# Performance work log

Hardware: AMD Instinct MI355X
Metric: run time of the kernel (lower is better)

Reference implementation:

```python
import jax, jax.numpy as jnp
import numpy as np

K = 20           # top_k
EPS_NORM = 1e-12  # F.normalize default eps


def setup_inputs() -> dict:
    key = jax.random.key(0)
    ks = jax.random.split(key, 16)
    B, C, R, S, SCB, ST, H = 8192, 3755, 214, 13, 30, 6, 64
    return {
        "char_logits": jax.random.normal(ks[0], (B, C), jnp.float32),
        "radical_logits": jax.random.normal(ks[1], (B, R), jnp.float32),
        "structure": jax.random.normal(ks[2], (B, S), jnp.float32),
        "stroke_count": jax.random.normal(ks[3], (B, SCB), jnp.float32),
        "stroke_types": jax.random.normal(ks[4], (B, ST), jnp.float32),
        "radical_mask": jax.random.randint(ks[5], (C, R), 0, 2, jnp.int32),
        "structure_label": jax.random.randint(ks[6], (C,), 0, S, jnp.int32),
        "stroke_count_label": jax.random.randint(ks[7], (C,), 0, SCB, jnp.int32),
        "stroke_type_sig": jax.random.uniform(ks[8], (C, ST), jnp.float32),
        "W1": jax.random.normal(ks[9], (6, H), jnp.float32) * 0.3,
        "b1": jax.random.normal(ks[10], (H,), jnp.float32) * 0.1,
        "W2": jax.random.normal(ks[11], (H, 1), jnp.float32) * 0.3,
        "b2": jax.random.normal(ks[12], (1,), jnp.float32) * 0.1,
        "reranker_weight": jnp.asarray(0.1, jnp.float32),
    }


def _features(char_logits, radical_logits, structure, stroke_count, stroke_types,
              radical_mask, structure_label, stroke_count_label, stroke_type_sig,
              top_idx):
    sg = jax.lax.stop_gradient
    # all model outputs except char_logits are detached by caller; char_logits
    # is detached inside _compute_features for the neural-confidence feature
    rl, st, sc, sty = sg(radical_logits), sg(structure), sg(stroke_count), sg(stroke_types)
    cl_d = sg(char_logits)

    # feature 1/2: radical match & false-alarm ratios
    radical_probs = jax.nn.sigmoid(rl)                              # (B, R)
    cand_mask = radical_mask[top_idx].astype(jnp.float32)           # (B, K, R)
    detected = jnp.einsum('br,bkr->bk', radical_probs, cand_mask)   # (B, K)
    cand_counts = jnp.maximum(cand_mask.sum(-1), 1.0)
    radical_match_ratio = detected / cand_counts
    total_prob = jnp.maximum(radical_probs.sum(-1, keepdims=True), 1e-6)  # (B,1)
    false_alarm_mass = radical_probs.sum(-1, keepdims=True) - detected
    radical_false_ratio = false_alarm_mass / total_prob

    # feature 3: structure match probability
    structure_probs = jax.nn.softmax(st, axis=-1)                   # (B, S)
    cand_structure = structure_label[top_idx]                       # (B, K)
    structure_match = jnp.take_along_axis(structure_probs, cand_structure, axis=1)

    # feature 4: normalized stroke-count distance
    stroke_pred = jnp.argmax(sc, axis=-1)                           # (B,)
    cand_stroke = stroke_count_label[top_idx]                       # (B, K)
    stroke_distance = jnp.abs(stroke_pred[:, None] - cand_stroke).astype(jnp.float32) / 29.0

    # feature 5: zero-masked stroke-type cosine
    cand_sig = stroke_type_sig[top_idx]                             # (B, K, 6)
    sig_norm_val = jnp.linalg.norm(cand_sig, axis=-1)               # (B, K)
    has_sig = (sig_norm_val > 1e-6).astype(jnp.float32)
    pred_norm = sty / jnp.maximum(jnp.linalg.norm(sty, axis=-1, keepdims=True), EPS_NORM)
    cand_adj = cand_sig + 1e-8 * (1.0 - has_sig)[..., None]
    cand_norm = cand_adj / jnp.maximum(jnp.linalg.norm(cand_adj, axis=-1, keepdims=True), EPS_NORM)
    stroke_type_cos = jnp.einsum('bd,bkd->bk', pred_norm, cand_norm) * has_sig

    # feature 6: detached neural confidence
    neural_probs = jax.nn.softmax(cl_d, axis=-1)                    # (B, C)
    neural_conf = jnp.take_along_axis(neural_probs, top_idx, axis=1)

    return jnp.stack([radical_match_ratio, radical_false_ratio, structure_match,
                      stroke_distance, stroke_type_cos, neural_conf], axis=-1)  # (B, K, 6)


def reference(char_logits, radical_logits, structure, stroke_count, stroke_types,
              radical_mask, structure_label, stroke_count_label, stroke_type_sig,
              W1, b1, W2, b2, reranker_weight):
    B = char_logits.shape[0]
    top_logits, top_idx = jax.lax.top_k(char_logits, K)             # (B, K)
    feats = _features(char_logits, radical_logits, structure, stroke_count,
                      stroke_types, radical_mask, structure_label,
                      stroke_count_label, stroke_type_sig, top_idx)
    h = jax.nn.relu(feats @ W1 + b1)                                # (B, K, H)
    rerank_scores = (h @ W2 + b2)[..., 0]                           # (B, K)
    combined_top = top_logits + reranker_weight * rerank_scores
    rows = jnp.arange(B)[:, None]
    return char_logits.at[rows, top_idx].set(combined_top)
```

## Files before the change

### kernel.cpp

```cpp
#include <hip/hip_runtime.h>
#include <math.h>

#define NB   8192
#define NC   3755
#define NR   214
#define NS   13
#define NSC  30
#define NST  6
#define NH   64
#define KTOP 20
#define RPB  4
#define NT   (RPB * 64)
#define NQT  15
#define NBIN 1024
#define CAP  192

__device__ __forceinline__ unsigned sortkey(float x) {
    unsigned u = __float_as_uint(x);
    return (u & 0x80000000u) ? ~u : (u | 0x80000000u);
}
__device__ __forceinline__ float inv_sortkey(unsigned k) {
    unsigned u = (k & 0x80000000u) ? (k ^ 0x80000000u) : ~k;
    return __uint_as_float(u);
}
__device__ __forceinline__ int lane_prefix(unsigned long long m) {
    int c = __builtin_amdgcn_mbcnt_lo((unsigned)m, 0);
    return __builtin_amdgcn_mbcnt_hi((unsigned)(m >> 32), c);
}

__global__ __launch_bounds__(256) void prep_kernel(
    const int* __restrict__ radical_mask,
    unsigned*  __restrict__ ws_bits)
{
    const int lane = threadIdx.x & 63;
    const int wave = threadIdx.x >> 6;
    const int c    = blockIdx.x * 4 + wave;
    if (c >= NC) return;
    unsigned long long bits[4];
#pragma unroll
    for (int i = 0; i < 4; ++i) {
        int r = lane + i * 64;
        bool pred = (r < NR) && (radical_mask[(size_t)c * NR + r] != 0);
        bits[i] = __ballot(pred);
    }
    if (lane == 0) {
        uint4 wa = make_uint4((unsigned)bits[0], (unsigned)(bits[0] >> 32),
                              (unsigned)bits[1], (unsigned)(bits[1] >> 32));
        uint4 wb = make_uint4((unsigned)bits[2], (unsigned)(bits[2] >> 32),
                              (unsigned)bits[3], (unsigned)(bits[3] >> 32));
        reinterpret_cast<uint4*>(ws_bits)[(size_t)c * 2 + 0] = wa;
        reinterpret_cast<uint4*>(ws_bits)[(size_t)c * 2 + 1] = wb;
    }
}

__global__ __launch_bounds__(NT, 8) void select_kernel(
    const float* __restrict__ char_logits,
    float*       __restrict__ out,
    float*       __restrict__ ws_topv,
    int*         __restrict__ ws_topi,
    float*       __restrict__ ws_stat)
{
    const int tid  = threadIdx.x;
    const int lane = tid & 63;
    const int wave = tid >> 6;
    const int row  = blockIdx.x * RPB + wave;

    __shared__ unsigned           s_hist32[RPB / 2][NBIN];
    __shared__ unsigned long long s_cand[RPB][CAP];
    __shared__ int s_cnt[RPB];
    __shared__ int s_need[RPB];

    const int      hw  = wave >> 1;
    const unsigned hsh = (wave & 1) * 16;

    const size_t rowOff = (size_t)row * NC;
    const float* __restrict__ rin  = char_logits + rowOff;
    float*       __restrict__ rout = out + rowOff;

    const int a     = (int)((4 - (rowOff & 3)) & 3);
    const int nq    = (NC - a) >> 2;
    const int ntail = NC - a - 4 * nq;

    int ext_idx = -1;
    if (lane < a)                           ext_idx = lane;
    else if (lane >= 8 && lane < 8 + ntail) ext_idx = a + 4 * nq + (lane - 8);

    const unsigned FLOORK = 0xC0000000u;
    float ext = -INFINITY;
    if (ext_idx >= 0) {
        ext = rin[ext_idx];
        rout[ext_idx] = ext;
    }
    float e0 = __expf(ext), e1 = 0.f, e2 = 0.f, e3 = 0.f;
    float m0 = ext, m1 = -INFINITY, m2 = -INFINITY, m3 = -INFINITY;
    int base = 0;

#pragma unroll
    for (int t = 0; t < 14; ++t) {
        const int q = lane + t * 64;
        float4 x = *reinterpret_cast<const float4*>(rin + a + 4 * q);
        *reinterpret_cast<float4*>(rout + a + 4 * q) = x;
        e0 += __expf(x.x); e1 += __expf(x.y);
        e2 += __expf(x.z); e3 += __expf(x.w);
        m0 = fmaxf(m0, x.x); m1 = fmaxf(m1, x.y);
        m2 = fmaxf(m2, x.z); m3 = fmaxf(m3, x.w);
        unsigned kk[4] = { sortkey(x.x), sortkey(x.y), sortkey(x.z), sortkey(x.w) };
#pragma unroll
        for (int j = 0; j < 4; ++j) {
            bool pred = kk[j] >= FLOORK;
            unsigned long long bal = __ballot(pred);
            if (pred) {
                int pos = base + lane_prefix(bal);
                if (pos < CAP)
                    s_cand[wave][pos] = ((unsigned long long)kk[j] << 32)
                                      | (0xFFFFFFFFu - (unsigned)(a + 4 * q + j));
            }
            base += (int)__popcll(bal);
        }
    }
    {
        const int q = lane + 896;
        const bool inb = q < nq;
        float4 x = make_float4(-INFINITY, -INFINITY, -INFINITY, -INFINITY);
        if (inb) {
            x = *reinterpret_cast<const float4*>(rin + a + 4 * q);
            *reinterpret_cast<float4*>(rout + a + 4 * q) = x;
        }
        e0 += __expf(x.x); e1 += __expf(x.y);
        e2 += __expf(x.z); e3 += __expf(x.w);
        m0 = fmaxf(m0, x.x); m1 = fmaxf(m1, x.y);
        m2 = fmaxf(m2, x.z); m3 = fmaxf(m3, x.w);
        unsigned kk[4] = { sortkey(x.x), sortkey(x.y), sortkey(x.z), sortkey(x.w) };
#pragma unroll
        for (int j = 0; j < 4; ++j) {
            bool pred = kk[j] >= FLOORK;
            unsigned long long bal = __ballot(pred);
            if (pred) {
                int pos = base + lane_prefix(bal);
                if (pos < CAP)
                    s_cand[wave][pos] = ((unsigned long long)kk[j] << 32)
                                      | (0xFFFFFFFFu - (unsigned)(a + 4 * q + j));
            }
            base += (int)__popcll(bal);
        }
    }
    {
        unsigned k = sortkey(ext);
        bool pred = k >= FLOORK;
        unsigned long long bal = __ballot(pred);
        if (pred) {
            int pos = base + lane_prefix(bal);
            if (pos < CAP)
                s_cand[wave][pos] = ((unsigned long long)k << 32)
                                  | (0xFFFFFFFFu - (unsigned)ext_idx);
        }
        base += (int)__popcll(bal);
    }

    float lmax = fmaxf(fmaxf(m0, m1), fmaxf(m2, m3));
#pragma unroll
    for (int off = 32; off > 0; off >>= 1) lmax = fmaxf(lmax, __shfl_xor(lmax, off));
    const float rowmax = lmax;
    float S = (e0 + e1) + (e2 + e3);
#pragma unroll
    for (int off = 32; off > 0; off >>= 1) S += __shfl_xor(S, off);

    int M = base;
    const bool ok = (M >= KTOP) && (M <= CAP) && (fabsf(rowmax) <= 60.f);
    float sumexp = S * __expf(-rowmax);
    if (lane == 0) s_need[wave] = ok ? 0 : 1;
    __syncthreads();
    const int any = s_need[0] | s_need[1] | s_need[2] | s_need[3];

    if (any) {
        const bool bad = !ok;
        for (int i = tid; i < (RPB / 2) * NBIN; i += NT)
            (&s_hist32[0][0])[i] = 0u;
        __syncthreads();
        if (bad) {
            if (ext_idx >= 0) atomicAdd(&s_hist32[hw][sortkey(ext) >> 22], 1u << hsh);
            for (int t = 0; t < NQT; ++t) {
                int q = lane + t * 64;
                if (q < nq) {
                    float4 x = *reinterpret_cast<const float4*>(rin + a + 4 * q);
                    atomicAdd(&s_hist32[hw][sortkey(x.x) >> 22], 1u << hsh);
                    atomicAdd(&s_hist32[hw][sortkey(x.y) >> 22], 1u << hsh);
                    atomicAdd(&s_hist32[hw][sortkey(x.z) >> 22], 1u << hsh);
                    atomicAdd(&s_hist32[hw][sortkey(x.w) >> 22], 1u << hsh);
                }
            }
        }
        __syncthreads();
        int B0 = 0;
        if (bad) {
            int bb = (int)(sortkey(rowmax) >> 22), cum = 0;
            while (bb >= 0) {
                cum += (int)((s_hist32[hw][bb] >> hsh) & 0xFFFFu);
                if (cum >= KTOP) break;
                --bb;
            }
            B0 = (bb < 0) ? 0 : bb;
            if (lane == 0) s_cnt[wave] = 0;
        }
        __syncthreads();
        if (bad) {
            float f0 = 0.f, f1 = 0.f, f2 = 0.f, f3 = 0.f;
            if (ext_idx >= 0) {
                f0 += __expf(ext - rowmax);
                unsigned k = sortkey(ext);
                if ((int)(k >> 22) >= B0) {
                    int pos = atomicAdd(&s_cnt[wave], 1);
                    if (pos < CAP)
                        s_cand[wave][pos] = ((unsigned long long)k << 32) | (0xFFFFFFFFu - (unsigned)ext_idx);
                }
            }
            for (int t = 0; t < NQT; ++t) {
                int q = lane + t * 64;
                if (q < nq) {
                    float4 x = *reinterpret_cast<const float4*>(rin + a + 4 * q);
                    f0 += __expf(x.x - rowmax); f1 += __expf(x.y - rowmax);
                    f2 += __expf(x.z - rowmax); f3 += __expf(x.w - rowmax);
                    unsigned kk[4] = { sortkey(x.x), sortkey(x.y), sortkey(x.z), sortkey(x.w) };
#pragma unroll
                    for (int j = 0; j < 4; ++j) {
                        if ((int)(kk[j] >> 22) >= B0) {
                            int pos = atomicAdd(&s_cnt[wave], 1);
                            if (pos < CAP)
                                s_cand[wave][pos] = ((unsigned long long)kk[j] << 32)
                                                  | (0xFFFFFFFFu - (unsigned)(a + 4 * q + j));
                        }
                    }
                }
            }
            float ls = (f0 + f1) + (f2 + f3);
#pragma unroll
            for (int off = 32; off > 0; off >>= 1) ls += __shfl_xor(ls, off);
            sumexp = ls;
            M = s_cnt[wave]; if (M > CAP) M = CAP;
        }
    }

    for (int c = lane; c < M; c += 64) {
        unsigned long long pc = s_cand[wave][c];
        int rank = 0;
        for (int j = 0; j < M; ++j) rank += (s_cand[wave][j] > pc) ? 1 : 0;
        if (rank < KTOP) {
            ws_topv[(size_t)row * KTOP + rank] = inv_sortkey((unsigned)(pc >> 32));
            ws_topi[(size_t)row * KTOP + rank] = (int)(0xFFFFFFFFu - (unsigned)(pc & 0xFFFFFFFFu));
        }
    }
    if (lane == 0) {
        ws_stat[2 * row + 0] = rowmax;
        ws_stat[2 * row + 1] = sumexp;
    }
}

__global__ __launch_bounds__(256, 8) void rerank_kernel(
    const float* __restrict__ radical_logits,
    const float* __restrict__ structure,
    const float* __restrict__ stroke_count,
    const float* __restrict__ stroke_types,
    const int*   __restrict__ structure_label,
    const int*   __restrict__ stroke_count_label,
    const float* __restrict__ stroke_type_sig,
    const float* __restrict__ W1,
    const float* __restrict__ b1,
    const float* __restrict__ W2,
    const float* __restrict__ b2,
    const float* __restrict__ rw,
    const float* __restrict__ ws_topv,
    const int*   __restrict__ ws_topi,
    const float* __restrict__ ws_stat,
    const unsigned* __restrict__ ws_bits,
    float*       __restrict__ out)
{
    const int row  = blockIdx.x;
    const int tid  = threadIdx.x;
    const int lane = tid & 63;
    const int wave = tid >> 6;

    __shared__ float s_probs[256];
    __shared__ float s_struct[NS];
    __shared__ float s_aux[8];
    __shared__ float s_topv[KTOP];
    __shared__ int   s_topi[KTOP];
    __shared__ float s_stat2[2];

    s_probs[tid] = (tid < NR)
        ? 1.f / (1.f + __expf(-radical_logits[(size_t)row * NR + tid])) : 0.f;
    if (tid < KTOP) {
        s_topv[tid] = ws_topv[(size_t)row * KTOP + tid];
        s_topi[tid] = ws_topi[(size_t)row * KTOP + tid];
    }
    if (tid == 216) {
        float sv[NS]; float m = -INFINITY;
#pragma unroll
        for (int i = 0; i < NS; ++i) { sv[i] = structure[(size_t)row * NS + i]; m = fmaxf(m, sv[i]); }
        float s = 0.f;
#pragma unroll
        for (int i = 0; i < NS; ++i) { sv[i] = __expf(sv[i] - m); s += sv[i]; }
        float inv = 1.f / s;
#pragma unroll
        for (int i = 0; i < NS; ++i) s_struct[i] = sv[i] * inv;
    } else if (tid == 217) {
        float bv = -INFINITY; int bi = 0;
#pragma unroll
        for (int i = 0; i < NSC; ++i) {
            float x = stroke_count[(size_t)row * NSC + i];
            if (x > bv) { bv = x; bi = i; }
        }
        s_aux[6] = (float)bi;
    } else if (tid == 218) {
        float t6[NST]; float ss = 0.f;
#pragma unroll
        for (int i = 0; i < NST; ++i) { t6[i] = stroke_types[(size_t)row * NST + i]; ss += t6[i] * t6[i]; }
        float inv = 1.f / fmaxf(sqrtf(ss), 1e-12f);
#pragma unroll
        for (int i = 0; i < NST; ++i) s_aux[i] = t6[i] * inv;
    } else if (tid == 219) {
        s_stat2[0] = ws_stat[2 * row + 0];
        s_stat2[1] = ws_stat[2 * row + 1];
    }
    __syncthreads();

    const float p0 = s_probs[lane];
    const float p1 = s_probs[lane + 64];
    const float p2 = s_probs[lane + 128];
    const float p3 = s_probs[lane + 192];
    float psum = p0 + p1 + p2 + p3;
#pragma unroll
    for (int off = 32; off > 0; off >>= 1) psum += __shfl_xor(psum, off);
    const float total = psum;

    const float rowmax = s_stat2[0];
    const float sumexp = s_stat2[1];
    const float b1v = b1[lane];
    float w1v[6];
#pragma unroll
    for (int j = 0; j < 6; ++j) w1v[j] = W1[j * NH + lane];
    const float w2v = W2[lane];
    const float b2v = b2[0];
    const float wrk = rw[0];
    const float spred = s_aux[6];
    const unsigned l5 = lane & 31;
    const bool hi = lane >= 32;

#pragma unroll
    for (int j = 0; j < KTOP / 4; ++j) {
        const int   k  = wave * (KTOP / 4) + j;
        const int   ci = __builtin_amdgcn_readfirstlane(s_topi[k]);
        const float tv = s_topv[k];

        const uint4* bq = reinterpret_cast<const uint4*>(ws_bits) + (size_t)ci * 2;
        const uint4 wa = bq[0], wb = bq[1];
        float cnt = (float)(__popc(wa.x) + __popc(wa.y) + __popc(wa.z) + __popc(wa.w)
                          + __popc(wb.x) + __popc(wb.y) + __popc(wb.z));
        float det = 0.f;
        det += ((( hi ? wa.y : wa.x) >> l5) & 1u) ? p0 : 0.f;
        det += ((( hi ? wa.w : wa.z) >> l5) & 1u) ? p1 : 0.f;
        det += ((( hi ? wb.y : wb.x) >> l5) & 1u) ? p2 : 0.f;
        det += ((( hi ? wb.w : wb.z) >> l5) & 1u) ? p3 : 0.f;
#pragma unroll
        for (int off = 32; off > 0; off >>= 1) det += __shfl_xor(det, off);

        float f1 = det / fmaxf(cnt, 1.f);
        float f2 = (total - det) / fmaxf(total, 1e-6f);
        float f3 = s_struct[structure_label[ci]];
        float f4 = fabsf(spred - (float)stroke_count_label[ci]) * (1.f / 29.f);
        float sig[NST]; float ss = 0.f;
#pragma unroll
        for (int i = 0; i < NST; ++i) { sig[i] = stroke_type_sig[(size_t)ci * NST + i]; ss += sig[i] * sig[i]; }
        float nrm = sqrtf(ss);
        float has = (nrm > 1e-6f) ? 1.f : 0.f;
        float add = 1e-8f * (1.f - has);
        float ss2 = 0.f;
#pragma unroll
        for (int i = 0; i < NST; ++i) { sig[i] += add; ss2 += sig[i] * sig[i]; }
        float inv = 1.f / fmaxf(sqrtf(ss2), 1e-12f);
        float dot = 0.f;
#pragma unroll
        for (int i = 0; i < NST; ++i) dot += s_aux[i] * sig[i] * inv;
        float f5 = dot * has;
        float f6 = __expf(tv - rowmax) / sumexp;

        float acc = b1v + f1 * w1v[0] + f2 * w1v[1] + f3 * w1v[2]
                        + f4 * w1v[3] + f5 * w1v[4] + f6 * w1v[5];
        float h = fmaxf(acc, 0.f);
        float part = h * w2v;
#pragma unroll
        for (int off = 32; off > 0; off >>= 1) part += __shfl_xor(part, off);
        if (lane == 0) out[(size_t)row * NC + ci] = tv + wrk * (part + b2v);
    }
}

extern "C" void kernel_launch(void* const* d_in, const int* in_sizes, int n_in,
                              void* d_out, int out_size, void* d_ws, size_t ws_size,
                              hipStream_t stream) {
    (void)in_sizes; (void)n_in; (void)out_size; (void)ws_size;
    const float* char_logits        = (const float*)d_in[0];
    const float* radical_logits     = (const float*)d_in[1];
    const float* structure          = (const float*)d_in[2];
    const float* stroke_count       = (const float*)d_in[3];
    const float* stroke_types       = (const float*)d_in[4];
    const int*   radical_mask       = (const int*)d_in[5];
    const int*   structure_label    = (const int*)d_in[6];
    const int*   stroke_count_label = (const int*)d_in[7];
    const float* stroke_type_sig    = (const float*)d_in[8];
    const float* W1                 = (const float*)d_in[9];
    const float* b1                 = (const float*)d_in[10];
    const float* W2                 = (const float*)d_in[11];
    const float* b2                 = (const float*)d_in[12];
    const float* rw                 = (const float*)d_in[13];
    float* out = (float*)d_out;

    float*    ws_topv = (float*)d_ws;
    int*      ws_topi = (int*)(ws_topv + (size_t)NB * KTOP);
    float*    ws_stat = (float*)(ws_topi + (size_t)NB * KTOP);
    unsigned* ws_bits = (unsigned*)(ws_stat + (size_t)NB * 2);

    prep_kernel<<<(NC + 3) / 4, 256, 0, stream>>>(radical_mask, ws_bits);
    select_kernel<<<NB / RPB, NT, 0, stream>>>(char_logits, out, ws_topv, ws_topi, ws_stat);
    rerank_kernel<<<NB, 256, 0, stream>>>(
        radical_logits, structure, stroke_count, stroke_types,
        structure_label, stroke_count_label, stroke_type_sig,
        W1, b1, W2, b2, rw, ws_topv, ws_topi, ws_stat, ws_bits, out);
}
```

Measured before the change: 384.7 us.

## Software-prefetch select loop, use LDS atomics for candidates, rerank four rows per block

In the select kernel, the fully unrolled copy/exp/candidate loop becomes a rolled loop that preloads the next float4 one iteration ahead. Candidate compaction now uses per-wave LDS atomicAdd counters in place of ballot/mbcnt prefix sums. The rerank kernel maps one row per wave, so four rows per block, with per-wave shared buffers and a quarter of the blocks. The aims are to overlap global loads, cut ballot overhead and cut block launch and sync cost. LDS atomics can serialise and break the ordered insertion, and dropping the unroll may hurt ILP.

```diff
diff --git a/kernel.cpp b/kernel.cpp
--- a/kernel.cpp
+++ b/kernel.cpp
@@ -23,10 +23,6 @@
     unsigned u = (k & 0x80000000u) ? (k ^ 0x80000000u) : ~k;
     return __uint_as_float(u);
 }
-__device__ __forceinline__ int lane_prefix(unsigned long long m) {
-    int c = __builtin_amdgcn_mbcnt_lo((unsigned)m, 0);
-    return __builtin_amdgcn_mbcnt_hi((unsigned)(m >> 32), c);
-}
 
 __global__ __launch_bounds__(256) void prep_kernel(
     const int* __restrict__ radical_mask,
@@ -85,6 +81,9 @@
     if (lane < a)                           ext_idx = lane;
     else if (lane >= 8 && lane < 8 + ntail) ext_idx = a + 4 * nq + (lane - 8);
 
+    if (tid < RPB) s_cnt[tid] = 0;
+    __syncthreads();
+
     const unsigned FLOORK = 0xC0000000u;
     float ext = -INFINITY;
     if (ext_idx >= 0) {
@@ -93,68 +92,44 @@
     }
     float e0 = __expf(ext), e1 = 0.f, e2 = 0.f, e3 = 0.f;
     float m0 = ext, m1 = -INFINITY, m2 = -INFINITY, m3 = -INFINITY;
-    int base = 0;
-
-#pragma unroll
-    for (int t = 0; t < 14; ++t) {
+
+    float4 nxt = make_float4(-INFINITY, -INFINITY, -INFINITY, -INFINITY);
+    if (lane < nq) nxt = *reinterpret_cast<const float4*>(rin + a + 4 * lane);
+
+    for (int t = 0; t < NQT; ++t) {
         const int q = lane + t * 64;
-        float4 x = *reinterpret_cast<const float4*>(rin + a + 4 * q);
-        *reinterpret_cast<float4*>(rout + a + 4 * q) = x;
-        e0 += __expf(x.x); e1 += __expf(x.y);
-        e2 += __expf(x.z); e3 += __expf(x.w);
-        m0 = fmaxf(m0, x.x); m1 = fmaxf(m1, x.y);
-        m2 = fmaxf(m2, x.z); m3 = fmaxf(m3, x.w);
-        unsigned kk[4] = { sortkey(x.x), sortkey(x.y), sortkey(x.z), sortkey(x.w) };
-#pragma unroll
-        for (int j = 0; j < 4; ++j) {
-            bool pred = kk[j] >= FLOORK;
-            unsigned long long bal = __ballot(pred);
-            if (pred) {
-                int pos = base + lane_prefix(bal);
-                if (pos < CAP)
-                    s_cand[wave][pos] = ((unsigned long long)kk[j] << 32)
-                                      | (0xFFFFFFFFu - (unsigned)(a + 4 * q + j));
+        const float4 x = nxt;
+        nxt = make_float4(-INFINITY, -INFINITY, -INFINITY, -INFINITY);
+        if (t + 1 < NQT) {
+            int qn = lane + (t + 1) * 64;
+            if (qn < nq) nxt = *reinterpret_cast<const float4*>(rin + a + 4 * qn);
+        }
+        if (q < nq) {
+            *reinterpret_cast<float4*>(rout + a + 4 * q) = x;
+            e0 += __expf(x.x); e1 += __expf(x.y);
+            e2 += __expf(x.z); e3 += __expf(x.w);
+            m0 = fmaxf(m0, x.x); m1 = fmaxf(m1, x.y);
+            m2 = fmaxf(m2, x.z); m3 = fmaxf(m3, x.w);
+            unsigned kk[4] = { sortkey(x.x), sortkey(x.y), sortkey(x.z), sortkey(x.w) };
+#pragma unroll
+            for (int j = 0; j < 4; ++j) {
+                if (kk[j] >= FLOORK) {
+                    int pos = atomicAdd(&s_cnt[wave], 1);
+                    if (pos < CAP)
+                        s_cand[wave][pos] = ((unsigned long long)kk[j] << 32)
+                                          | (0xFFFFFFFFu - (unsigned)(a + 4 * q + j));
+                }
             }
-            base += (int)__popcll(bal);
-        }
-    }
-    {
-        const int q = lane + 896;
-        const bool inb = q < nq;
-        float4 x = make_float4(-INFINITY, -INFINITY, -INFINITY, -INFINITY);
-        if (inb) {
-            x = *reinterpret_cast<const float4*>(rin + a + 4 * q);
-            *reinterpret_cast<float4*>(rout + a + 4 * q) = x;
-        }
-        e0 += __expf(x.x); e1 += __expf(x.y);
-        e2 += __expf(x.z); e3 += __expf(x.w);
-        m0 = fmaxf(m0, x.x); m1 = fmaxf(m1, x.y);
-        m2 = fmaxf(m2, x.z); m3 = fmaxf(m3, x.w);
-        unsigned kk[4] = { sortkey(x.x), sortkey(x.y), sortkey(x.z), sortkey(x.w) };
-#pragma unroll
-        for (int j = 0; j < 4; ++j) {
-            bool pred = kk[j] >= FLOORK;
-            unsigned long long bal = __ballot(pred);
-            if (pred) {
-                int pos = base + lane_prefix(bal);
-                if (pos < CAP)
-                    s_cand[wave][pos] = ((unsigned long long)kk[j] << 32)
-                                      | (0xFFFFFFFFu - (unsigned)(a + 4 * q + j));
-            }
-            base += (int)__popcll(bal);
-        }
-    }
-    {
+        }
+    }
+    if (ext_idx >= 0) {
         unsigned k = sortkey(ext);
-        bool pred = k >= FLOORK;
-        unsigned long long bal = __ballot(pred);
-        if (pred) {
-            int pos = base + lane_prefix(bal);
+        if (k >= FLOORK) {
+            int pos = atomicAdd(&s_cnt[wave], 1);
             if (pos < CAP)
                 s_cand[wave][pos] = ((unsigned long long)k << 32)
                                   | (0xFFFFFFFFu - (unsigned)ext_idx);
         }
-        base += (int)__popcll(bal);
     }
 
     float lmax = fmaxf(fmaxf(m0, m1), fmaxf(m2, m3));
@@ -165,7 +140,7 @@
 #pragma unroll
     for (int off = 32; off > 0; off >>= 1) S += __shfl_xor(S, off);
 
-    int M = base;
+    int M = s_cnt[wave];
     const bool ok = (M >= KTOP) && (M <= CAP) && (fabsf(rowmax) <= 60.f);
     float sumexp = S * __expf(-rowmax);
     if (lane == 0) s_need[wave] = ok ? 0 : 1;
@@ -274,25 +249,31 @@
     const unsigned* __restrict__ ws_bits,
     float*       __restrict__ out)
 {
-    const int row  = blockIdx.x;
     const int tid  = threadIdx.x;
     const int lane = tid & 63;
     const int wave = tid >> 6;
-
-    __shared__ float s_probs[256];
-    __shared__ float s_struct[NS];
-    __shared__ float s_aux[8];
-    __shared__ float s_topv[KTOP];
-    __shared__ int   s_topi[KTOP];
-    __shared__ float s_stat2[2];
-
-    s_probs[tid] = (tid < NR)
-        ? 1.f / (1.f + __expf(-radical_logits[(size_t)row * NR + tid])) : 0.f;
-    if (tid < KTOP) {
-        s_topv[tid] = ws_topv[(size_t)row * KTOP + tid];
-        s_topi[tid] = ws_topi[(size_t)row * KTOP + tid];
-    }
-    if (tid == 216) {
+    const int row  = blockIdx.x * 4 + wave;
+
+    __shared__ float s_probs[4][256];
+    __shared__ float s_struct[4][NS];
+    __shared__ float s_aux[4][8];
+    __shared__ float s_topv[4][KTOP];
+    __shared__ int   s_topi[4][KTOP];
+    __shared__ float s_stat2[4][2];
+
+#pragma unroll
+    for (int i = 0; i < 4; ++i) {
+        int r = lane + i * 64;
+        s_probs[wave][r] = (r < NR)
+            ? 1.f / (1.f + __expf(-radical_logits[(size_t)row * NR + r])) : 0.f;
+    }
+    if (lane < KTOP) {
+        s_topv[wave][lane] = ws_topv[(size_t)row * KTOP + lane];
+        s_topi[wave][lane] = ws_topi[(size_t)row * KTOP + lane];
+    } else if (lane == 24) {
+        s_stat2[wave][0] = ws_stat[2 * row + 0];
+        s_stat2[wave][1] = ws_stat[2 * row + 1];
+    } else if (lane == 25) {
         float sv[NS]; float m = -INFINITY;
 #pragma unroll
         for (int i = 0; i < NS; ++i) { sv[i] = structure[(size_t)row * NS + i]; m = fmaxf(m, sv[i]); }
@@ -301,39 +282,36 @@
         for (int i = 0; i < NS; ++i) { sv[i] = __expf(sv[i] - m); s += sv[i]; }
         float inv = 1.f / s;
 #pragma unroll
-        for (int i = 0; i < NS; ++i) s_struct[i] = sv[i] * inv;
-    } else if (tid == 217) {
+        for (int i = 0; i < NS; ++i) s_struct[wave][i] = sv[i] * inv;
+    } else if (lane == 26) {
         float bv = -INFINITY; int bi = 0;
 #pragma unroll
         for (int i = 0; i < NSC; ++i) {
             float x = stroke_count[(size_t)row * NSC + i];
             if (x > bv) { bv = x; bi = i; }
         }
-        s_aux[6] = (float)bi;
-    } else if (tid == 218) {
+        s_aux[wave][6] = (float)bi;
+    } else if (lane == 27) {
         float t6[NST]; float ss = 0.f;
 #pragma unroll
         for (int i = 0; i < NST; ++i) { t6[i] = stroke_types[(size_t)row * NST + i]; ss += t6[i] * t6[i]; }
         float inv = 1.f / fmaxf(sqrtf(ss), 1e-12f);
 #pragma unroll
-        for (int i = 0; i < NST; ++i) s_aux[i] = t6[i] * inv;
-    } else if (tid == 219) {
-        s_stat2[0] = ws_stat[2 * row + 0];
-        s_stat2[1] = ws_stat[2 * row + 1];
+        for (int i = 0; i < NST; ++i) s_aux[wave][i] = t6[i] * inv;
     }
     __syncthreads();
 
-    const float p0 = s_probs[lane];
-    const float p1 = s_probs[lane + 64];
-    const float p2 = s_probs[lane + 128];
-    const float p3 = s_probs[lane + 192];
+    const float p0 = s_probs[wave][lane];
+    const float p1 = s_probs[wave][lane + 64];
+    const float p2 = s_probs[wave][lane + 128];
+    const float p3 = s_probs[wave][lane + 192];
     float psum = p0 + p1 + p2 + p3;
 #pragma unroll
     for (int off = 32; off > 0; off >>= 1) psum += __shfl_xor(psum, off);
     const float total = psum;
 
-    const float rowmax = s_stat2[0];
-    const float sumexp = s_stat2[1];
+    const float rowmax = s_stat2[wave][0];
+    const float sumexp = s_stat2[wave][1];
     const float b1v = b1[lane];
     float w1v[6];
 #pragma unroll
@@ -341,15 +319,13 @@
     const float w2v = W2[lane];
     const float b2v = b2[0];
     const float wrk = rw[0];
-    const float spred = s_aux[6];
+    const float spred = s_aux[wave][6];
     const unsigned l5 = lane & 31;
     const bool hi = lane >= 32;
 
-#pragma unroll
-    for (int j = 0; j < KTOP / 4; ++j) {
-        const int   k  = wave * (KTOP / 4) + j;
-        const int   ci = __builtin_amdgcn_readfirstlane(s_topi[k]);
-        const float tv = s_topv[k];
+    for (int k = 0; k < KTOP; ++k) {
+        const int   ci = __builtin_amdgcn_readfirstlane(s_topi[wave][k]);
+        const float tv = s_topv[wave][k];
 
         const uint4* bq = reinterpret_cast<const uint4*>(ws_bits) + (size_t)ci * 2;
         const uint4 wa = bq[0], wb = bq[1];
@@ -365,7 +341,7 @@
 
         float f1 = det / fmaxf(cnt, 1.f);
         float f2 = (total - det) / fmaxf(total, 1e-6f);
-        float f3 = s_struct[structure_label[ci]];
+        float f3 = s_struct[wave][structure_label[ci]];
         float f4 = fabsf(spred - (float)stroke_count_label[ci]) * (1.f / 29.f);
         float sig[NST]; float ss = 0.f;
 #pragma unroll
@@ -379,7 +355,7 @@
         float inv = 1.f / fmaxf(sqrtf(ss2), 1e-12f);
         float dot = 0.f;
 #pragma unroll
-        for (int i = 0; i < NST; ++i) dot += s_aux[i] * sig[i] * inv;
+        for (int i = 0; i < NST; ++i) dot += s_aux[wave][i] * sig[i] * inv;
         float f5 = dot * has;
         float f6 = __expf(tv - rowmax) / sumexp;
 
@@ -420,7 +396,7 @@
 
     prep_kernel<<<(NC + 3) / 4, 256, 0, stream>>>(radical_mask, ws_bits);
     select_kernel<<<NB / RPB, NT, 0, stream>>>(char_logits, out, ws_topv, ws_topi, ws_stat);
-    rerank_kernel<<<NB, 256, 0, stream>>>(
+    rerank_kernel<<<NB / 4, 256, 0, stream>>>(
         radical_logits, structure, stroke_count, stroke_types,
         structure_label, stroke_count_label, stroke_type_sig,
         W1, b1, W2, b2, rw, ws_topv, ws_topi, ws_stat, ws_bits, out);
```

Measured after the change: 338.9 us. -11.9%, faster.
